# Performance work log

Hardware: AMD Instinct MI355X
Metric: run time of the kernel (lower is better)

The kernel has to match this reference:

```python
import jax, jax.numpy as jnp
import numpy as np

N, E, D_IN, H, L, B, D_OUT = 50000, 800000, 128, 128, 3, 512, 64
BN_EPS = 1e-5


def _leaky(v):
    return jax.nn.leaky_relu(v, 0.2)


def _bn_eval(v, g, b):
    # eval-mode BatchNorm1d with running_mean=0, running_var=1
    return g * v * (1.0 / np.sqrt(1.0 + BN_EPS)) + b


def setup_inputs() -> dict:
    key = jax.random.key(0)
    ks = jax.random.split(key, 12)
    s = 0.02  # weight init scale
    return {
        "x": jax.random.normal(ks[0], (N, D_IN), jnp.float32),
        "edge_index": jax.random.randint(ks[1], (2, E), 0, N, jnp.int64),
        "batch": jnp.sort(jax.random.randint(ks[2], (N,), 0, B, jnp.int64)),
        "node_W": jax.random.normal(ks[3], (D_IN, H), jnp.float32) * s,
        "node_b": jnp.zeros((H,), jnp.float32),
        "conv_W1": jax.random.normal(ks[4], (L, H, H), jnp.float32) * s,
        "conv_b1": jnp.zeros((L, H), jnp.float32),
        "conv_g": jnp.ones((L, H), jnp.float32),
        "conv_beta": jnp.zeros((L, H), jnp.float32),
        "conv_W2": jax.random.normal(ks[5], (L, H, H), jnp.float32) * s,
        "conv_b2": jnp.zeros((L, H), jnp.float32),
        "vn_emb": jax.random.normal(ks[6], (1, H), jnp.float32) * s,
        "vn_W1": jax.random.normal(ks[7], (L, H, H), jnp.float32) * s,
        "vn_b1": jnp.zeros((L, H), jnp.float32),
        "vn_W2": jax.random.normal(ks[8], (L, H, H), jnp.float32) * s,
        "vn_b2": jnp.zeros((L, H), jnp.float32),
        "bn_g": jnp.ones((H,), jnp.float32),
        "bn_b": jnp.zeros((H,), jnp.float32),
        "fc_W": jax.random.normal(ks[9], (D_OUT, H), jnp.float32) * s,
        "fc_b": jnp.zeros((D_OUT,), jnp.float32),
    }


def reference(x, edge_index, batch, node_W, node_b, conv_W1, conv_b1, conv_g,
              conv_beta, conv_W2, conv_b2, vn_emb, vn_W1, vn_b1, vn_W2, vn_b2,
              bn_g, bn_b, fc_W, fc_b):
    src, dst = edge_index[0], edge_index[1]
    h = x @ node_W + node_b                              # [N, H]
    vn = jnp.broadcast_to(vn_emb, (B, vn_emb.shape[1]))  # [B, H]
    counts = jax.ops.segment_sum(jnp.ones((h.shape[0],), h.dtype), batch,
                                 num_segments=B)          # [B]
    denom = jnp.maximum(counts, 1.0)[:, None]
    for l in range(L):
        h = h + vn[batch]
        # GINConv (eps=0): mlp((1+eps)*x + sum of neighbor messages)
        agg = jax.ops.segment_sum(h[src], dst, num_segments=h.shape[0])
        z = h + agg
        z = _leaky(z @ conv_W1[l] + conv_b1[l])
        z = _bn_eval(z, conv_g[l], conv_beta[l])
        h = _leaky(z @ conv_W2[l] + conv_b2[l])
        # dropout is identity in eval mode
        vn_update = jax.ops.segment_sum(h, batch, num_segments=B) / denom
        vn = vn + (_leaky(vn_update @ vn_W1[l] + vn_b1[l]) @ vn_W2[l] + vn_b2[l])
    out = jax.ops.segment_sum(h, batch, num_segments=B)   # global_add_pool
    out = _bn_eval(out, bn_g, bn_b)
    return out @ fc_W.T + fc_b                            # [B, D_OUT]
```

## Files before the change

kernel.cpp:

```cpp
#include <hip/hip_runtime.h>
#include <hip/hip_bf16.h>

#define NN 50000
#define NE 800000
#define NB 512
#define WT_S 136
#define WT_M (128 * WT_S)
#define DCAP 64

using u32 = unsigned int;
using u16 = unsigned short;
typedef __attribute__((ext_vector_type(8))) short short8;
typedef __attribute__((ext_vector_type(4))) float f32x4;

constexpr float BNS = 0.9999950000374998f;

__device__ inline u16 f2bf(float f) {
    u32 b = __builtin_bit_cast(u32, f);
    return (u16)((b + 0x7FFFu + ((b >> 16) & 1u)) >> 16);
}
__device__ inline float bf2f(u32 u) {
    return __builtin_bit_cast(float, u << 16);
}
__device__ inline u32 pk2(float a, float b) {
    return (u32)f2bf(a) | ((u32)f2bf(b) << 16);
}

__global__ void k_wprep(const float* __restrict__ nW, const float* __restrict__ cW1,
                        const float* __restrict__ cW2, u16* __restrict__ wt) {
    int idx = blockIdx.x * 256 + threadIdx.x;
    int m = idx >> 14, e = idx & 16383;
    int k = e >> 7, c = e & 127;
    const float* src = m == 0 ? nW : (m <= 3 ? cW1 + (m - 1) * 16384 : cW2 + (m - 4) * 16384);
    wt[m * WT_M + c * WT_S + k] = f2bf(src[e]);
}

__global__ void k_setup(const float* __restrict__ vn_emb, float* __restrict__ vn,
                        u16* __restrict__ vnb, const int* __restrict__ batch,
                        int* __restrict__ bstart, float* __restrict__ counts) {
    int idx = blockIdx.x * 256 + threadIdx.x;
    if (idx < NB * 128) {
        float v = vn_emb[idx & 127];
        vn[idx] = v;
        vnb[idx] = f2bf(v);
    }
    if (idx <= NB) {
        int b = idx;
        int lo = 0, hi = NN;
        while (lo < hi) { int m = (lo + hi) >> 1; if (batch[m] < b) lo = m + 1; else hi = m; }
        bstart[b] = lo;
        if (b < NB) {
            int b1 = b + 1, lo1 = 0, hi1 = NN;
            while (lo1 < hi1) { int m = (lo1 + hi1) >> 1; if (batch[m] < b1) lo1 = m + 1; else hi1 = m; }
            counts[b] = (float)(lo1 - lo);
        }
    }
}

__global__ void k_pcsr(const int* __restrict__ ei, const int* __restrict__ batch,
                       int* __restrict__ deg, u32* __restrict__ nbr) {
    int e = blockIdx.x * 256 + threadIdx.x;
    if (e >= NE) return;
    int src = ei[e];
    int dst = ei[NE + e];
    int pos = atomicAdd(&deg[dst], 1);
    if (pos < DCAP) nbr[(size_t)dst * DCAP + pos] = (u32)src | ((u32)batch[src] << 16);
}

__global__ __launch_bounds__(256) void k_gather(
    const int* __restrict__ deg, const u32* __restrict__ nbr,
    const u16* __restrict__ hb0, const u16* __restrict__ vnb,
    const int* __restrict__ batch, u16* __restrict__ ah, u16* __restrict__ alo) {
    int node = blockIdx.x * 8 + (threadIdx.x >> 5);
    int q = threadIdx.x & 31;
    if (node >= NN) return;
    const uint2* h2 = (const uint2*)hb0;
    const uint2* v2 = (const uint2*)vnb;
    const u32* nb = nbr + (size_t)node * DCAP;
    int n = min(deg[node], DCAP);
    uint2 vd = h2[(size_t)node * 32 + q];
    uint2 wd = v2[(size_t)batch[node] * 32 + q];
    float4 A = {bf2f(vd.x & 0xFFFFu) + bf2f(wd.x & 0xFFFFu),
                bf2f(vd.x >> 16) + bf2f(wd.x >> 16),
                bf2f(vd.y & 0xFFFFu) + bf2f(wd.y & 0xFFFFu),
                bf2f(vd.y >> 16) + bf2f(wd.y >> 16)};
    float4 Bc = {0.f, 0.f, 0.f, 0.f};
    int j = 0;
    for (; j + 3 < n; j += 4) {
        uint4 nn = *(const uint4*)(nb + j);
        uint2 u0 = h2[(size_t)(nn.x & 0xFFFFu) * 32 + q];
        uint2 w0 = v2[(size_t)(nn.x >> 16) * 32 + q];
        uint2 u1 = h2[(size_t)(nn.y & 0xFFFFu) * 32 + q];
        uint2 w1 = v2[(size_t)(nn.y >> 16) * 32 + q];
        uint2 u2 = h2[(size_t)(nn.z & 0xFFFFu) * 32 + q];
        uint2 w2 = v2[(size_t)(nn.z >> 16) * 32 + q];
        uint2 u3 = h2[(size_t)(nn.w & 0xFFFFu) * 32 + q];
        uint2 w3 = v2[(size_t)(nn.w >> 16) * 32 + q];
        A.x += bf2f(u0.x & 0xFFFFu) + bf2f(w0.x & 0xFFFFu);
        A.y += bf2f(u0.x >> 16) + bf2f(w0.x >> 16);
        A.z += bf2f(u0.y & 0xFFFFu) + bf2f(w0.y & 0xFFFFu);
        A.w += bf2f(u0.y >> 16) + bf2f(w0.y >> 16);
        Bc.x += bf2f(u1.x & 0xFFFFu) + bf2f(w1.x & 0xFFFFu);
        Bc.y += bf2f(u1.x >> 16) + bf2f(w1.x >> 16);
        Bc.z += bf2f(u1.y & 0xFFFFu) + bf2f(w1.y & 0xFFFFu);
        Bc.w += bf2f(u1.y >> 16) + bf2f(w1.y >> 16);
        A.x += bf2f(u2.x & 0xFFFFu) + bf2f(w2.x & 0xFFFFu);
        A.y += bf2f(u2.x >> 16) + bf2f(w2.x >> 16);
        A.z += bf2f(u2.y & 0xFFFFu) + bf2f(w2.y & 0xFFFFu);
        A.w += bf2f(u2.y >> 16) + bf2f(w2.y >> 16);
        Bc.x += bf2f(u3.x & 0xFFFFu) + bf2f(w3.x & 0xFFFFu);
        Bc.y += bf2f(u3.x >> 16) + bf2f(w3.x >> 16);
        Bc.z += bf2f(u3.y & 0xFFFFu) + bf2f(w3.y & 0xFFFFu);
        Bc.w += bf2f(u3.y >> 16) + bf2f(w3.y >> 16);
    }
    for (; j < n; ++j) {
        u32 nn = nb[j];
        uint2 u0 = h2[(size_t)(nn & 0xFFFFu) * 32 + q];
        uint2 w0 = v2[(size_t)(nn >> 16) * 32 + q];
        A.x += bf2f(u0.x & 0xFFFFu) + bf2f(w0.x & 0xFFFFu);
        A.y += bf2f(u0.x >> 16) + bf2f(w0.x >> 16);
        A.z += bf2f(u0.y & 0xFFFFu) + bf2f(w0.y & 0xFFFFu);
        A.w += bf2f(u0.y >> 16) + bf2f(w0.y >> 16);
    }
    A.x += Bc.x; A.y += Bc.y; A.z += Bc.z; A.w += Bc.w;
    u16 h0 = f2bf(A.x), h1 = f2bf(A.y), h2_ = f2bf(A.z), h3 = f2bf(A.w);
    ((uint2*)ah)[(size_t)node * 32 + q] =
        make_uint2((u32)h0 | ((u32)h1 << 16), (u32)h2_ | ((u32)h3 << 16));
    ((uint2*)alo)[(size_t)node * 32 + q] =
        make_uint2(pk2(A.x - bf2f(h0), A.y - bf2f(h1)),
                   pk2(A.z - bf2f(h2_), A.w - bf2f(h3)));
}

template <int EPI, int AMODE, bool OBF16>
__global__ __launch_bounds__(512) void k_gemm(
    const void* __restrict__ Ap, const void* __restrict__ Ap2,
    const u16* __restrict__ wt, const float* __restrict__ bias,
    const float* __restrict__ gg, const float* __restrict__ bb,
    void* __restrict__ outp, int nrows) {
    __shared__ u16 sW[WT_M];
    const int t = threadIdx.x;
    {
        const float4* src = (const float4*)wt;
        float4* dst = (float4*)sW;
        for (int i = t; i < WT_M / 8; i += 512) dst[i] = src[i];
    }
    __syncthreads();
    const int lane = t & 63;
    const int w = t >> 6;
    const int rl = lane & 15;
    const int q = lane >> 4;
    const int rbase = blockIdx.x * 256 + w * 32;

    short8 af[2][4], al[2][4];
#pragma unroll
    for (int ri = 0; ri < 2; ++ri) {
        int row = min(rbase + ri * 16 + rl, nrows - 1);
#pragma unroll
        for (int kc = 0; kc < 4; ++kc) {
            if (AMODE == 2) {
                const float* ap = (const float*)Ap + (size_t)row * 128 + kc * 32 + q * 8;
                float4 f0 = *(const float4*)ap;
                float4 f1 = *(const float4*)(ap + 4);
                float fv[8] = {f0.x, f0.y, f0.z, f0.w, f1.x, f1.y, f1.z, f1.w};
                short8 hi, lo;
#pragma unroll
                for (int i = 0; i < 8; ++i) {
                    u16 hv = f2bf(fv[i]);
                    hi[i] = (short)hv;
                    lo[i] = (short)f2bf(fv[i] - bf2f(hv));
                }
                af[ri][kc] = hi;
                al[ri][kc] = lo;
            } else {
                af[ri][kc] = *(const short8*)((const u16*)Ap + (size_t)row * 128 + kc * 32 + q * 8);
                if (AMODE == 1)
                    al[ri][kc] = *(const short8*)((const u16*)Ap2 + (size_t)row * 128 + kc * 32 + q * 8);
            }
        }
    }

#pragma unroll
    for (int ct = 0; ct < 8; ++ct) {
        f32x4 acc0 = {0.f, 0.f, 0.f, 0.f};
        f32x4 acc1 = {0.f, 0.f, 0.f, 0.f};
#pragma unroll
        for (int kc = 0; kc < 4; ++kc) {
            short8 bf = *(const short8*)&sW[(ct * 16 + rl) * WT_S + kc * 32 + q * 8];
            if (AMODE != 0) {
                acc0 = __builtin_amdgcn_mfma_f32_16x16x32_bf16(al[0][kc], bf, acc0, 0, 0, 0);
                acc1 = __builtin_amdgcn_mfma_f32_16x16x32_bf16(al[1][kc], bf, acc1, 0, 0, 0);
            }
            acc0 = __builtin_amdgcn_mfma_f32_16x16x32_bf16(af[0][kc], bf, acc0, 0, 0, 0);
            acc1 = __builtin_amdgcn_mfma_f32_16x16x32_bf16(af[1][kc], bf, acc1, 0, 0, 0);
        }
        const int col = ct * 16 + rl;
        const float bs = bias[col];
        const float g = (EPI == 2) ? gg[col] : 0.f;
        const float be = (EPI == 2) ? bb[col] : 0.f;
#pragma unroll
        for (int half = 0; half < 2; ++half) {
            const f32x4& ac = half ? acc1 : acc0;
#pragma unroll
            for (int i = 0; i < 4; ++i) {
                int r = rbase + half * 16 + q * 4 + i;
                if (r < nrows) {
                    float v = ac[i] + bs;
                    if (EPI >= 1) v = v > 0.f ? v : 0.2f * v;
                    if (EPI == 2) v = g * v * BNS + be;
                    if (OBF16) ((u16*)outp)[(size_t)r * 128 + col] = f2bf(v);
                    else ((float*)outp)[(size_t)r * 128 + col] = v;
                }
            }
        }
    }
}

__global__ __launch_bounds__(256) void k_vnup(
    const u16* __restrict__ hb0, const int* __restrict__ bstart,
    const float* __restrict__ counts, const float* __restrict__ W1,
    const float* __restrict__ b1, const float* __restrict__ W2,
    const float* __restrict__ b2, float* __restrict__ vn, u16* __restrict__ vnb) {
    __shared__ float4 red[8][32];
    __shared__ float sP[128], sT[128], sH[2][128];
    const int b = blockIdx.x;
    const int t = threadIdx.x;
    const int s = bstart[b], e = bstart[b + 1];
    const int g = t >> 5, q = t & 31;
    const uint2* h2 = (const uint2*)hb0;
    float4 a = make_float4(0.f, 0.f, 0.f, 0.f);
    for (int r = s + g; r < e; r += 8) {
        uint2 v = h2[(size_t)r * 32 + q];
        a.x += bf2f(v.x & 0xFFFFu); a.y += bf2f(v.x >> 16);
        a.z += bf2f(v.y & 0xFFFFu); a.w += bf2f(v.y >> 16);
    }
    red[g][q] = a;
    __syncthreads();
    if (g == 0) {
#pragma unroll
        for (int g2 = 1; g2 < 8; ++g2) {
            float4 v = red[g2][q];
            a.x += v.x; a.y += v.y; a.z += v.z; a.w += v.w;
        }
        float inv = 1.f / fmaxf(counts[b], 1.f);
        sP[q * 4 + 0] = a.x * inv;
        sP[q * 4 + 1] = a.y * inv;
        sP[q * 4 + 2] = a.z * inv;
        sP[q * 4 + 3] = a.w * inv;
    }
    __syncthreads();
    {
        const int c = t & 127, hf = t >> 7;
        float acc = 0.f;
        const float* Wp = W1 + (size_t)(hf * 64) * 128 + c;
#pragma unroll 8
        for (int k = 0; k < 64; ++k) acc += sP[hf * 64 + k] * Wp[(size_t)k * 128];
        sH[hf][c] = acc;
    }
    __syncthreads();
    if (t < 128) {
        float v = sH[0][t] + sH[1][t] + b1[t];
        sT[t] = v > 0.f ? v : 0.2f * v;
    }
    __syncthreads();
    {
        const int c = t & 127, hf = t >> 7;
        float acc = 0.f;
        const float* Wp = W2 + (size_t)(hf * 64) * 128 + c;
#pragma unroll 8
        for (int k = 0; k < 64; ++k) acc += sT[hf * 64 + k] * Wp[(size_t)k * 128];
        sH[hf][c] = acc;
    }
    __syncthreads();
    if (t < 128) {
        float nv = vn[(size_t)b * 128 + t] + sH[0][t] + sH[1][t] + b2[t];
        vn[(size_t)b * 128 + t] = nv;
        vnb[(size_t)b * 128 + t] = f2bf(nv);
    }
}

__global__ __launch_bounds__(256) void k_final(
    const u16* __restrict__ hb0, const int* __restrict__ bstart,
    const float* __restrict__ g, const float* __restrict__ bB,
    const float* __restrict__ fcW, const float* __restrict__ fcb,
    float* __restrict__ out) {
    __shared__ float sP[4][128];
    __shared__ float4 red[4][2][32];
    const int t = threadIdx.x;
    const int seg = t >> 6, gq = t & 63, rg = gq >> 5, q = gq & 31;
    const int b = blockIdx.x * 4 + seg;
    const int s = bstart[b], e = bstart[b + 1];
    const uint2* h2 = (const uint2*)hb0;
    float4 a = make_float4(0.f, 0.f, 0.f, 0.f);
    for (int r = s + rg; r < e; r += 2) {
        uint2 v = h2[(size_t)r * 32 + q];
        a.x += bf2f(v.x & 0xFFFFu); a.y += bf2f(v.x >> 16);
        a.z += bf2f(v.y & 0xFFFFu); a.w += bf2f(v.y >> 16);
    }
    red[seg][rg][q] = a;
    __syncthreads();
    if (rg == 0) {
        float4 v = red[seg][1][q];
        a.x += v.x; a.y += v.y; a.z += v.z; a.w += v.w;
        float av[4] = {a.x, a.y, a.z, a.w};
#pragma unroll
        for (int i = 0; i < 4; ++i) {
            int c = q * 4 + i;
            sP[seg][c] = g[c] * av[i] * BNS + bB[c];
        }
    }
    __syncthreads();
    const int o = t & 63;
    float acc = fcb[o];
    const float* wrow = fcW + o * 128;
    const float* prow = sP[seg];
    for (int k = 0; k < 128; ++k) acc += prow[k] * wrow[k];
    out[(size_t)b * 64 + o] = acc;
}

extern "C" void kernel_launch(void* const* d_in, const int* in_sizes, int n_in,
                              void* d_out, int out_size, void* d_ws, size_t ws_size,
                              hipStream_t stream) {
    const float* x       = (const float*)d_in[0];
    const int*   ei      = (const int*)d_in[1];
    const int*   batch   = (const int*)d_in[2];
    const float* node_W  = (const float*)d_in[3];
    const float* node_b  = (const float*)d_in[4];
    const float* conv_W1 = (const float*)d_in[5];
    const float* conv_b1 = (const float*)d_in[6];
    const float* conv_g  = (const float*)d_in[7];
    const float* conv_bt = (const float*)d_in[8];
    const float* conv_W2 = (const float*)d_in[9];
    const float* conv_b2 = (const float*)d_in[10];
    const float* vn_emb  = (const float*)d_in[11];
    const float* vn_W1   = (const float*)d_in[12];
    const float* vn_b1   = (const float*)d_in[13];
    const float* vn_W2   = (const float*)d_in[14];
    const float* vn_b2   = (const float*)d_in[15];
    const float* bn_g    = (const float*)d_in[16];
    const float* bn_b    = (const float*)d_in[17];
    const float* fc_W    = (const float*)d_in[18];
    const float* fc_b    = (const float*)d_in[19];
    float* out = (float*)d_out;

    char* ws = (char*)d_ws;
    u16* hb0   = (u16*)ws;
    u16* aggh  = hb0 + (size_t)NN * 128;
    u16* agglo = aggh + (size_t)NN * 128;
    u16* wt    = agglo + (size_t)NN * 128;
    u32* nbr   = (u32*)(wt + 7 * WT_M);
    float* vn  = (float*)(nbr + (size_t)NN * DCAP);
    u16* vnb   = (u16*)(vn + NB * 128);
    float* counts = (float*)(vnb + NB * 128);
    int* bstart = (int*)(counts + NB);
    int* deg    = bstart + NB + 1;

    hipMemsetAsync(deg, 0, NN * sizeof(int), stream);
    k_wprep<<<448, 256, 0, stream>>>(node_W, conv_W1, conv_W2, wt);
    k_pcsr<<<(NE + 255) / 256, 256, 0, stream>>>(ei, batch, deg, nbr);
    k_setup<<<(NB * 128 + 255) / 256, 256, 0, stream>>>(vn_emb, vn, vnb, batch, bstart, counts);

    const int GG = (NN + 255) / 256;

    k_gemm<0, 2, true><<<GG, 512, 0, stream>>>(
        x, nullptr, wt, node_b, nullptr, nullptr, hb0, NN);

    for (int l = 0; l < 3; ++l) {
        k_gather<<<(NN + 7) / 8, 256, 0, stream>>>(deg, nbr, hb0, vnb, batch, aggh, agglo);
        k_gemm<2, 1, true><<<GG, 512, 0, stream>>>(
            aggh, agglo, wt + (size_t)(1 + l) * WT_M, conv_b1 + l * 128,
            conv_g + l * 128, conv_bt + l * 128, aggh, NN);
        k_gemm<1, 0, true><<<GG, 512, 0, stream>>>(
            aggh, nullptr, wt + (size_t)(4 + l) * WT_M, conv_b2 + l * 128,
            nullptr, nullptr, hb0, NN);
        if (l < 2)
            k_vnup<<<NB, 256, 0, stream>>>(hb0, bstart, counts, vn_W1 + l * 16384,
                                           vn_b1 + l * 128, vn_W2 + l * 16384,
                                           vn_b2 + l * 128, vn, vnb);
    }

    k_final<<<NB / 4, 256, 0, stream>>>(hb0, bstart, bn_g, bn_b, fc_W, fc_b, out);
}
```

Baseline: 348.0 us.

## Partition edges by destination slice before building padded neighbor lists

Replaces the single scattered CSR build with a two-pass partition. Edges are first bucketed into 8 destination slices using block histograms, a scan and a scatter. A fill kernel then processes each slice with its own group of blocks, so the deg atomics and nbr writes stay within a localized region intended to be cache friendly. The weight-prep and setup kernels are also merged into one launch. This adds three extra launches and an extra pass over the edges. The fill order is also tied to the slice-to-block mapping, which may interact with L2/XCD locality.

After: 358.6 us. 3.0% more time.

```diff
diff --git a/kernel.cpp b/kernel.cpp
--- a/kernel.cpp
+++ b/kernel.cpp
@@ -7,6 +7,11 @@
 #define WT_S 136
 #define WT_M (128 * WT_S)
 #define DCAP 64
+#define NSL 8
+#define SLW 6250
+#define PCH 2048
+#define PBK ((NE + PCH - 1) / PCH)
+#define BPS 112
 
 using u32 = unsigned int;
 using u16 = unsigned short;
@@ -26,19 +31,20 @@
     return (u32)f2bf(a) | ((u32)f2bf(b) << 16);
 }
 
-__global__ void k_wprep(const float* __restrict__ nW, const float* __restrict__ cW1,
-                        const float* __restrict__ cW2, u16* __restrict__ wt) {
-    int idx = blockIdx.x * 256 + threadIdx.x;
-    int m = idx >> 14, e = idx & 16383;
-    int k = e >> 7, c = e & 127;
-    const float* src = m == 0 ? nW : (m <= 3 ? cW1 + (m - 1) * 16384 : cW2 + (m - 4) * 16384);
-    wt[m * WT_M + c * WT_S + k] = f2bf(src[e]);
-}
-
-__global__ void k_setup(const float* __restrict__ vn_emb, float* __restrict__ vn,
-                        u16* __restrict__ vnb, const int* __restrict__ batch,
-                        int* __restrict__ bstart, float* __restrict__ counts) {
-    int idx = blockIdx.x * 256 + threadIdx.x;
+__global__ void k_prep(const float* __restrict__ nW, const float* __restrict__ cW1,
+                       const float* __restrict__ cW2, u16* __restrict__ wt,
+                       const float* __restrict__ vn_emb, float* __restrict__ vn,
+                       u16* __restrict__ vnb, const int* __restrict__ batch,
+                       int* __restrict__ bstart, float* __restrict__ counts) {
+    if (blockIdx.x < 448) {
+        int idx = blockIdx.x * 256 + threadIdx.x;
+        int m = idx >> 14, e = idx & 16383;
+        int k = e >> 7, c = e & 127;
+        const float* src = m == 0 ? nW : (m <= 3 ? cW1 + (m - 1) * 16384 : cW2 + (m - 4) * 16384);
+        wt[m * WT_M + c * WT_S + k] = f2bf(src[e]);
+        return;
+    }
+    int idx = (blockIdx.x - 448) * 256 + threadIdx.x;
     if (idx < NB * 128) {
         float v = vn_emb[idx & 127];
         vn[idx] = v;
@@ -57,14 +63,82 @@
     }
 }
 
-__global__ void k_pcsr(const int* __restrict__ ei, const int* __restrict__ batch,
-                       int* __restrict__ deg, u32* __restrict__ nbr) {
-    int e = blockIdx.x * 256 + threadIdx.x;
-    if (e >= NE) return;
-    int src = ei[e];
-    int dst = ei[NE + e];
-    int pos = atomicAdd(&deg[dst], 1);
-    if (pos < DCAP) nbr[(size_t)dst * DCAP + pos] = (u32)src | ((u32)batch[src] << 16);
+__global__ __launch_bounds__(256) void k_part1(const int* __restrict__ ei,
+                                               int* __restrict__ blkcnt) {
+    __shared__ int hist[NSL];
+    const int t = threadIdx.x;
+    if (t < NSL) hist[t] = 0;
+    __syncthreads();
+    int base = blockIdx.x * PCH + t * 8;
+#pragma unroll
+    for (int i = 0; i < 8; ++i) {
+        int e = base + i;
+        if (e < NE) atomicAdd(&hist[ei[NE + e] / SLW], 1);
+    }
+    __syncthreads();
+    if (t < NSL) blkcnt[t * PBK + blockIdx.x] = hist[t];
+}
+
+__global__ __launch_bounds__(512) void k_pscan(const int* __restrict__ blkcnt,
+                                               int* __restrict__ blkofs,
+                                               int* __restrict__ sinfo) {
+    __shared__ int s[NSL * PBK];
+    __shared__ int tot[NSL], gb[NSL];
+    const int t = threadIdx.x;
+    for (int i = t; i < NSL * PBK; i += 512) s[i] = blkcnt[i];
+    __syncthreads();
+    if (t < NSL) {
+        int run = 0;
+        for (int b = 0; b < PBK; ++b) { int v = s[t * PBK + b]; s[t * PBK + b] = run; run += v; }
+        tot[t] = run;
+    }
+    __syncthreads();
+    if (t == 0) {
+        int run = 0;
+        for (int i = 0; i < NSL; ++i) { gb[i] = run; run += tot[i]; }
+    }
+    __syncthreads();
+    for (int i = t; i < NSL * PBK; i += 512) blkofs[i] = gb[i / PBK] + s[i];
+    if (t < NSL) { sinfo[t] = gb[t]; sinfo[NSL + t] = tot[t]; }
+}
+
+__global__ __launch_bounds__(256) void k_part2(const int* __restrict__ ei,
+                                               const int* __restrict__ blkofs,
+                                               u32* __restrict__ part) {
+    __shared__ int cur[NSL];
+    const int t = threadIdx.x;
+    if (t < NSL) cur[t] = blkofs[t * PBK + blockIdx.x];
+    __syncthreads();
+    int base = blockIdx.x * PCH + t * 8;
+#pragma unroll
+    for (int i = 0; i < 8; ++i) {
+        int e = base + i;
+        if (e < NE) {
+            int dst = ei[NE + e];
+            int src = ei[e];
+            int sl = dst / SLW;
+            int pos = atomicAdd(&cur[sl], 1);
+            part[pos] = (u32)src | ((u32)(dst - sl * SLW) << 16);
+        }
+    }
+}
+
+__global__ __launch_bounds__(256) void k_pfill(const u32* __restrict__ part,
+                                               const int* __restrict__ sinfo,
+                                               const int* __restrict__ batch,
+                                               int* __restrict__ deg, u32* __restrict__ nbr) {
+    const int sl = blockIdx.x & (NSL - 1);
+    const int sub = blockIdx.x >> 3;
+    const int base = sinfo[sl], cnt = sinfo[NSL + sl];
+    const int chunk = (cnt + BPS - 1) / BPS;
+    const int lo = sub * chunk, hi = min(lo + chunk, cnt);
+    for (int i = lo + (int)threadIdx.x; i < hi; i += 256) {
+        u32 v = part[base + i];
+        int src = (int)(v & 0xFFFFu);
+        int dst = sl * SLW + (int)(v >> 16);
+        int pos = atomicAdd(&deg[dst], 1);
+        if (pos < DCAP) nbr[(size_t)dst * DCAP + pos] = (u32)src | ((u32)batch[src] << 16);
+    }
 }
 
 __global__ __launch_bounds__(256) void k_gather(
@@ -348,16 +422,23 @@
     u16* agglo = aggh + (size_t)NN * 128;
     u16* wt    = agglo + (size_t)NN * 128;
     u32* nbr   = (u32*)(wt + 7 * WT_M);
-    float* vn  = (float*)(nbr + (size_t)NN * DCAP);
+    u32* part  = nbr + (size_t)NN * DCAP;
+    int* blkcnt = (int*)(part + NE);
+    int* blkofs = blkcnt + NSL * PBK;
+    int* sinfo  = blkofs + NSL * PBK;
+    float* vn  = (float*)(sinfo + 2 * NSL);
     u16* vnb   = (u16*)(vn + NB * 128);
     float* counts = (float*)(vnb + NB * 128);
     int* bstart = (int*)(counts + NB);
     int* deg    = bstart + NB + 1;
 
     hipMemsetAsync(deg, 0, NN * sizeof(int), stream);
-    k_wprep<<<448, 256, 0, stream>>>(node_W, conv_W1, conv_W2, wt);
-    k_pcsr<<<(NE + 255) / 256, 256, 0, stream>>>(ei, batch, deg, nbr);
-    k_setup<<<(NB * 128 + 255) / 256, 256, 0, stream>>>(vn_emb, vn, vnb, batch, bstart, counts);
+    k_prep<<<704, 256, 0, stream>>>(node_W, conv_W1, conv_W2, wt,
+                                    vn_emb, vn, vnb, batch, bstart, counts);
+    k_part1<<<PBK, 256, 0, stream>>>(ei, blkcnt);
+    k_pscan<<<1, 512, 0, stream>>>(blkcnt, blkofs, sinfo);
+    k_part2<<<PBK, 256, 0, stream>>>(ei, blkofs, part);
+    k_pfill<<<NSL * BPS, 256, 0, stream>>>(part, sinfo, batch, deg, nbr);
 
     const int GG = (NN + 255) / 256;
 
```

## Store node features in feature-sliced layout and partition gather by slice for cache locality

Applied to the files above, without the earlier changes.

Node embeddings and virtual-node embeddings are stored transposed into four 32-feature slices, so each slice of all nodes is contiguous. The gather kernel is restructured so each block handles one feature slice for half the nodes, with two lanes splitting the neighbor list and combining through a shuffle. This aims to shrink the working set per pass so random neighbor reads hit in L2/MALL. The setup and weight-prep kernels are also merged into one launch. The GEMM epilogue now writes scattered 2-byte stores into the sliced layout, which costs some write coalescing.

Result: slower. 365.9 us, median of 3 (+5.1%).

```diff
diff --git a/kernel.cpp b/kernel.cpp
--- a/kernel.cpp
+++ b/kernel.cpp
@@ -4,6 +4,7 @@
 #define NN 50000
 #define NE 800000
 #define NB 512
+#define HNN 25000
 #define WT_S 136
 #define WT_M (128 * WT_S)
 #define DCAP 64
@@ -26,23 +27,26 @@
     return (u32)f2bf(a) | ((u32)f2bf(b) << 16);
 }
 
-__global__ void k_wprep(const float* __restrict__ nW, const float* __restrict__ cW1,
-                        const float* __restrict__ cW2, u16* __restrict__ wt) {
-    int idx = blockIdx.x * 256 + threadIdx.x;
-    int m = idx >> 14, e = idx & 16383;
-    int k = e >> 7, c = e & 127;
-    const float* src = m == 0 ? nW : (m <= 3 ? cW1 + (m - 1) * 16384 : cW2 + (m - 4) * 16384);
-    wt[m * WT_M + c * WT_S + k] = f2bf(src[e]);
-}
-
-__global__ void k_setup(const float* __restrict__ vn_emb, float* __restrict__ vn,
-                        u16* __restrict__ vnb, const int* __restrict__ batch,
-                        int* __restrict__ bstart, float* __restrict__ counts) {
-    int idx = blockIdx.x * 256 + threadIdx.x;
+
+__global__ void k_prep(const float* __restrict__ nW, const float* __restrict__ cW1,
+                       const float* __restrict__ cW2, u16* __restrict__ wt,
+                       const float* __restrict__ vn_emb, float* __restrict__ vn,
+                       u16* __restrict__ vnbT, const int* __restrict__ batch,
+                       int* __restrict__ bstart, float* __restrict__ counts) {
+    if (blockIdx.x < 448) {
+        int idx = blockIdx.x * 256 + threadIdx.x;
+        int m = idx >> 14, e = idx & 16383;
+        int k = e >> 7, c = e & 127;
+        const float* src = m == 0 ? nW : (m <= 3 ? cW1 + (m - 1) * 16384 : cW2 + (m - 4) * 16384);
+        wt[m * WT_M + c * WT_S + k] = f2bf(src[e]);
+        return;
+    }
+    int idx = (blockIdx.x - 448) * 256 + threadIdx.x;
     if (idx < NB * 128) {
-        float v = vn_emb[idx & 127];
+        int b = idx >> 7, c = idx & 127;
+        float v = vn_emb[c];
         vn[idx] = v;
-        vnb[idx] = f2bf(v);
+        vnbT[((size_t)(c >> 5) * NB + b) * 32 + (c & 31)] = f2bf(v);
     }
     if (idx <= NB) {
         int b = idx;
@@ -69,74 +73,105 @@
 
 __global__ __launch_bounds__(256) void k_gather(
     const int* __restrict__ deg, const u32* __restrict__ nbr,
-    const u16* __restrict__ hb0, const u16* __restrict__ vnb,
+    const u16* __restrict__ hbT, const u16* __restrict__ vnbT,
     const int* __restrict__ batch, u16* __restrict__ ah, u16* __restrict__ alo) {
-    int node = blockIdx.x * 8 + (threadIdx.x >> 5);
-    int q = threadIdx.x & 31;
-    if (node >= NN) return;
-    const uint2* h2 = (const uint2*)hb0;
-    const uint2* v2 = (const uint2*)vnb;
-    const u32* nb = nbr + (size_t)node * DCAP;
-    int n = min(deg[node], DCAP);
-    uint2 vd = h2[(size_t)node * 32 + q];
-    uint2 wd = v2[(size_t)batch[node] * 32 + q];
-    float4 A = {bf2f(vd.x & 0xFFFFu) + bf2f(wd.x & 0xFFFFu),
-                bf2f(vd.x >> 16) + bf2f(wd.x >> 16),
-                bf2f(vd.y & 0xFFFFu) + bf2f(wd.y & 0xFFFFu),
-                bf2f(vd.y >> 16) + bf2f(wd.y >> 16)};
-    float4 Bc = {0.f, 0.f, 0.f, 0.f};
-    int j = 0;
-    for (; j + 3 < n; j += 4) {
-        uint4 nn = *(const uint4*)(nb + j);
-        uint2 u0 = h2[(size_t)(nn.x & 0xFFFFu) * 32 + q];
-        uint2 w0 = v2[(size_t)(nn.x >> 16) * 32 + q];
-        uint2 u1 = h2[(size_t)(nn.y & 0xFFFFu) * 32 + q];
-        uint2 w1 = v2[(size_t)(nn.y >> 16) * 32 + q];
-        uint2 u2 = h2[(size_t)(nn.z & 0xFFFFu) * 32 + q];
-        uint2 w2 = v2[(size_t)(nn.z >> 16) * 32 + q];
-        uint2 u3 = h2[(size_t)(nn.w & 0xFFFFu) * 32 + q];
-        uint2 w3 = v2[(size_t)(nn.w >> 16) * 32 + q];
-        A.x += bf2f(u0.x & 0xFFFFu) + bf2f(w0.x & 0xFFFFu);
-        A.y += bf2f(u0.x >> 16) + bf2f(w0.x >> 16);
-        A.z += bf2f(u0.y & 0xFFFFu) + bf2f(w0.y & 0xFFFFu);
-        A.w += bf2f(u0.y >> 16) + bf2f(w0.y >> 16);
-        Bc.x += bf2f(u1.x & 0xFFFFu) + bf2f(w1.x & 0xFFFFu);
-        Bc.y += bf2f(u1.x >> 16) + bf2f(w1.x >> 16);
-        Bc.z += bf2f(u1.y & 0xFFFFu) + bf2f(w1.y & 0xFFFFu);
-        Bc.w += bf2f(u1.y >> 16) + bf2f(w1.y >> 16);
-        A.x += bf2f(u2.x & 0xFFFFu) + bf2f(w2.x & 0xFFFFu);
-        A.y += bf2f(u2.x >> 16) + bf2f(w2.x >> 16);
-        A.z += bf2f(u2.y & 0xFFFFu) + bf2f(w2.y & 0xFFFFu);
-        A.w += bf2f(u2.y >> 16) + bf2f(w2.y >> 16);
-        Bc.x += bf2f(u3.x & 0xFFFFu) + bf2f(w3.x & 0xFFFFu);
-        Bc.y += bf2f(u3.x >> 16) + bf2f(w3.x >> 16);
-        Bc.z += bf2f(u3.y & 0xFFFFu) + bf2f(w3.y & 0xFFFFu);
-        Bc.w += bf2f(u3.y >> 16) + bf2f(w3.y >> 16);
-    }
-    for (; j < n; ++j) {
-        u32 nn = nb[j];
-        uint2 u0 = h2[(size_t)(nn & 0xFFFFu) * 32 + q];
-        uint2 w0 = v2[(size_t)(nn >> 16) * 32 + q];
-        A.x += bf2f(u0.x & 0xFFFFu) + bf2f(w0.x & 0xFFFFu);
-        A.y += bf2f(u0.x >> 16) + bf2f(w0.x >> 16);
-        A.z += bf2f(u0.y & 0xFFFFu) + bf2f(w0.y & 0xFFFFu);
-        A.w += bf2f(u0.y >> 16) + bf2f(w0.y >> 16);
-    }
-    A.x += Bc.x; A.y += Bc.y; A.z += Bc.z; A.w += Bc.w;
-    u16 h0 = f2bf(A.x), h1 = f2bf(A.y), h2_ = f2bf(A.z), h3 = f2bf(A.w);
-    ((uint2*)ah)[(size_t)node * 32 + q] =
-        make_uint2((u32)h0 | ((u32)h1 << 16), (u32)h2_ | ((u32)h3 << 16));
-    ((uint2*)alo)[(size_t)node * 32 + q] =
-        make_uint2(pk2(A.x - bf2f(h0), A.y - bf2f(h1)),
-                   pk2(A.z - bf2f(h2_), A.w - bf2f(h3)));
-}
-
-template <int EPI, int AMODE, bool OBF16>
+    const int s = blockIdx.x & 7;
+    const int sub = blockIdx.x >> 3;
+    const int f = s & 3;
+    const int hs = s >> 2;
+    const int lane = threadIdx.x & 63;
+    const int w = threadIdx.x >> 6;
+    const int g = lane >> 3, sl = lane & 7;
+    const int pair = sl >> 2, fl = sl & 3;
+    const int local = sub * 32 + w * 8 + g;
+    if (local >= HNN) return;
+    const int node = hs * HNN + local;
+
+    const uint4* hT = (const uint4*)hbT + (size_t)f * NN * 4;
+    const uint4* vT = (const uint4*)vnbT + (size_t)f * NB * 4;
+    const u32* nbp = nbr + (size_t)node * DCAP;
+    const int n = min(deg[node], DCAP);
+
+    float acc[8];
+    if (pair == 0) {
+        uint4 hv = hT[(size_t)node * 4 + fl];
+        uint4 vv = vT[(size_t)batch[node] * 4 + fl];
+        acc[0] = bf2f(hv.x & 0xFFFFu) + bf2f(vv.x & 0xFFFFu);
+        acc[1] = bf2f(hv.x >> 16) + bf2f(vv.x >> 16);
+        acc[2] = bf2f(hv.y & 0xFFFFu) + bf2f(vv.y & 0xFFFFu);
+        acc[3] = bf2f(hv.y >> 16) + bf2f(vv.y >> 16);
+        acc[4] = bf2f(hv.z & 0xFFFFu) + bf2f(vv.z & 0xFFFFu);
+        acc[5] = bf2f(hv.z >> 16) + bf2f(vv.z >> 16);
+        acc[6] = bf2f(hv.w & 0xFFFFu) + bf2f(vv.w & 0xFFFFu);
+        acc[7] = bf2f(hv.w >> 16) + bf2f(vv.w >> 16);
+    } else {
+#pragma unroll
+        for (int i = 0; i < 8; ++i) acc[i] = 0.f;
+    }
+
+    int j = pair;
+    for (; j + 2 < n; j += 4) {
+        u32 e0 = nbp[j], e1 = nbp[j + 2];
+        uint4 h0 = hT[(size_t)(e0 & 0xFFFFu) * 4 + fl];
+        uint4 v0 = vT[(size_t)(e0 >> 16) * 4 + fl];
+        uint4 h1 = hT[(size_t)(e1 & 0xFFFFu) * 4 + fl];
+        uint4 v1 = vT[(size_t)(e1 >> 16) * 4 + fl];
+        acc[0] += bf2f(h0.x & 0xFFFFu) + bf2f(v0.x & 0xFFFFu);
+        acc[1] += bf2f(h0.x >> 16) + bf2f(v0.x >> 16);
+        acc[2] += bf2f(h0.y & 0xFFFFu) + bf2f(v0.y & 0xFFFFu);
+        acc[3] += bf2f(h0.y >> 16) + bf2f(v0.y >> 16);
+        acc[4] += bf2f(h0.z & 0xFFFFu) + bf2f(v0.z & 0xFFFFu);
+        acc[5] += bf2f(h0.z >> 16) + bf2f(v0.z >> 16);
+        acc[6] += bf2f(h0.w & 0xFFFFu) + bf2f(v0.w & 0xFFFFu);
+        acc[7] += bf2f(h0.w >> 16) + bf2f(v0.w >> 16);
+        acc[0] += bf2f(h1.x & 0xFFFFu) + bf2f(v1.x & 0xFFFFu);
+        acc[1] += bf2f(h1.x >> 16) + bf2f(v1.x >> 16);
+        acc[2] += bf2f(h1.y & 0xFFFFu) + bf2f(v1.y & 0xFFFFu);
+        acc[3] += bf2f(h1.y >> 16) + bf2f(v1.y >> 16);
+        acc[4] += bf2f(h1.z & 0xFFFFu) + bf2f(v1.z & 0xFFFFu);
+        acc[5] += bf2f(h1.z >> 16) + bf2f(v1.z >> 16);
+        acc[6] += bf2f(h1.w & 0xFFFFu) + bf2f(v1.w & 0xFFFFu);
+        acc[7] += bf2f(h1.w >> 16) + bf2f(v1.w >> 16);
+    }
+    if (j < n) {
+        u32 e0 = nbp[j];
+        uint4 h0 = hT[(size_t)(e0 & 0xFFFFu) * 4 + fl];
+        uint4 v0 = vT[(size_t)(e0 >> 16) * 4 + fl];
+        acc[0] += bf2f(h0.x & 0xFFFFu) + bf2f(v0.x & 0xFFFFu);
+        acc[1] += bf2f(h0.x >> 16) + bf2f(v0.x >> 16);
+        acc[2] += bf2f(h0.y & 0xFFFFu) + bf2f(v0.y & 0xFFFFu);
+        acc[3] += bf2f(h0.y >> 16) + bf2f(v0.y >> 16);
+        acc[4] += bf2f(h0.z & 0xFFFFu) + bf2f(v0.z & 0xFFFFu);
+        acc[5] += bf2f(h0.z >> 16) + bf2f(v0.z >> 16);
+        acc[6] += bf2f(h0.w & 0xFFFFu) + bf2f(v0.w & 0xFFFFu);
+        acc[7] += bf2f(h0.w >> 16) + bf2f(v0.w >> 16);
+    }
+
+#pragma unroll
+    for (int i = 0; i < 8; ++i) acc[i] += __shfl_xor(acc[i], 4);
+
+    if (pair == 0) {
+        u16 hi[8];
+#pragma unroll
+        for (int i = 0; i < 8; ++i) hi[i] = f2bf(acc[i]);
+        uint4 ho = {(u32)hi[0] | ((u32)hi[1] << 16), (u32)hi[2] | ((u32)hi[3] << 16),
+                    (u32)hi[4] | ((u32)hi[5] << 16), (u32)hi[6] | ((u32)hi[7] << 16)};
+        uint4 lo = {pk2(acc[0] - bf2f(hi[0]), acc[1] - bf2f(hi[1])),
+                    pk2(acc[2] - bf2f(hi[2]), acc[3] - bf2f(hi[3])),
+                    pk2(acc[4] - bf2f(hi[4]), acc[5] - bf2f(hi[5])),
+                    pk2(acc[6] - bf2f(hi[6]), acc[7] - bf2f(hi[7]))};
+        const size_t oi = (size_t)node * 16 + f * 4 + fl;
+        ((uint4*)ah)[oi] = ho;
+        ((uint4*)alo)[oi] = lo;
+    }
+}
+
+template <int EPI, int AMODE, int OMODE>
 __global__ __launch_bounds__(512) void k_gemm(
     const void* __restrict__ Ap, const void* __restrict__ Ap2,
     const u16* __restrict__ wt, const float* __restrict__ bias,
     const float* __restrict__ gg, const float* __restrict__ bb,
-    void* __restrict__ outp, int nrows) {
+    u16* __restrict__ outp, int nrows) {
     __shared__ u16 sW[WT_M];
     const int t = threadIdx.x;
     {
@@ -207,8 +242,10 @@
                     float v = ac[i] + bs;
                     if (EPI >= 1) v = v > 0.f ? v : 0.2f * v;
                     if (EPI == 2) v = g * v * BNS + be;
-                    if (OBF16) ((u16*)outp)[(size_t)r * 128 + col] = f2bf(v);
-                    else ((float*)outp)[(size_t)r * 128 + col] = v;
+                    if (OMODE == 0)
+                        outp[(size_t)r * 128 + col] = f2bf(v);
+                    else
+                        outp[((size_t)(col >> 5) * NN + r) * 32 + (col & 31)] = f2bf(v);
                 }
             }
         }
@@ -216,20 +253,22 @@
 }
 
 __global__ __launch_bounds__(256) void k_vnup(
-    const u16* __restrict__ hb0, const int* __restrict__ bstart,
+    const u16* __restrict__ hbT, const int* __restrict__ bstart,
     const float* __restrict__ counts, const float* __restrict__ W1,
     const float* __restrict__ b1, const float* __restrict__ W2,
-    const float* __restrict__ b2, float* __restrict__ vn, u16* __restrict__ vnb) {
+    const float* __restrict__ b2, float* __restrict__ vn, u16* __restrict__ vnbT) {
     __shared__ float4 red[8][32];
     __shared__ float sP[128], sT[128], sH[2][128];
     const int b = blockIdx.x;
     const int t = threadIdx.x;
     const int s = bstart[b], e = bstart[b + 1];
     const int g = t >> 5, q = t & 31;
-    const uint2* h2 = (const uint2*)hb0;
+    const uint2* h2 = (const uint2*)hbT;
+    const size_t fbase = (size_t)(q >> 3) * NN * 8;
+    const int fo = q & 7;
     float4 a = make_float4(0.f, 0.f, 0.f, 0.f);
     for (int r = s + g; r < e; r += 8) {
-        uint2 v = h2[(size_t)r * 32 + q];
+        uint2 v = h2[fbase + (size_t)r * 8 + fo];
         a.x += bf2f(v.x & 0xFFFFu); a.y += bf2f(v.x >> 16);
         a.z += bf2f(v.y & 0xFFFFu); a.w += bf2f(v.y >> 16);
     }
@@ -274,12 +313,12 @@
     if (t < 128) {
         float nv = vn[(size_t)b * 128 + t] + sH[0][t] + sH[1][t] + b2[t];
         vn[(size_t)b * 128 + t] = nv;
-        vnb[(size_t)b * 128 + t] = f2bf(nv);
+        vnbT[((size_t)(t >> 5) * NB + b) * 32 + (t & 31)] = f2bf(nv);
     }
 }
 
 __global__ __launch_bounds__(256) void k_final(
-    const u16* __restrict__ hb0, const int* __restrict__ bstart,
+    const u16* __restrict__ hbT, const int* __restrict__ bstart,
     const float* __restrict__ g, const float* __restrict__ bB,
     const float* __restrict__ fcW, const float* __restrict__ fcb,
     float* __restrict__ out) {
@@ -289,10 +328,12 @@
     const int seg = t >> 6, gq = t & 63, rg = gq >> 5, q = gq & 31;
     const int b = blockIdx.x * 4 + seg;
     const int s = bstart[b], e = bstart[b + 1];
-    const uint2* h2 = (const uint2*)hb0;
+    const uint2* h2 = (const uint2*)hbT;
+    const size_t fbase = (size_t)(q >> 3) * NN * 8;
+    const int fo = q & 7;
     float4 a = make_float4(0.f, 0.f, 0.f, 0.f);
     for (int r = s + rg; r < e; r += 2) {
-        uint2 v = h2[(size_t)r * 32 + q];
+        uint2 v = h2[fbase + (size_t)r * 8 + fo];
         a.x += bf2f(v.x & 0xFFFFu); a.y += bf2f(v.x >> 16);
         a.z += bf2f(v.y & 0xFFFFu); a.w += bf2f(v.y >> 16);
     }
@@ -343,40 +384,41 @@
     float* out = (float*)d_out;
 
     char* ws = (char*)d_ws;
-    u16* hb0   = (u16*)ws;
-    u16* aggh  = hb0 + (size_t)NN * 128;
+    u16* hbT   = (u16*)ws;
+    u16* aggh  = hbT + (size_t)NN * 128;
     u16* agglo = aggh + (size_t)NN * 128;
     u16* wt    = agglo + (size_t)NN * 128;
     u32* nbr   = (u32*)(wt + 7 * WT_M);
     float* vn  = (float*)(nbr + (size_t)NN * DCAP);
-    u16* vnb   = (u16*)(vn + NB * 128);
-    float* counts = (float*)(vnb + NB * 128);
+    u16* vnbT  = (u16*)(vn + NB * 128);
+    float* counts = (float*)(vnbT + NB * 128);
     int* bstart = (int*)(counts + NB);
     int* deg    = bstart + NB + 1;
 
     hipMemsetAsync(deg, 0, NN * sizeof(int), stream);
-    k_wprep<<<448, 256, 0, stream>>>(node_W, conv_W1, conv_W2, wt);
+    k_prep<<<704, 256, 0, stream>>>(node_W, conv_W1, conv_W2, wt,
+                                    vn_emb, vn, vnbT, batch, bstart, counts);
     k_pcsr<<<(NE + 255) / 256, 256, 0, stream>>>(ei, batch, deg, nbr);
-    k_setup<<<(NB * 128 + 255) / 256, 256, 0, stream>>>(vn_emb, vn, vnb, batch, bstart, counts);
 
     const int GG = (NN + 255) / 256;
-
-    k_gemm<0, 2, true><<<GG, 512, 0, stream>>>(
-        x, nullptr, wt, node_b, nullptr, nullptr, hb0, NN);
+    const int GGA = 8 * ((HNN + 31) / 32);
+
+    k_gemm<0, 2, 1><<<GG, 512, 0, stream>>>(
+        x, nullptr, wt, node_b, nullptr, nullptr, hbT, NN);
 
     for (int l = 0; l < 3; ++l) {
-        k_gather<<<(NN + 7) / 8, 256, 0, stream>>>(deg, nbr, hb0, vnb, batch, aggh, agglo);
-        k_gemm<2, 1, true><<<GG, 512, 0, stream>>>(
+        k_gather<<<GGA, 256, 0, stream>>>(deg, nbr, hbT, vnbT, batch, aggh, agglo);
+        k_gemm<2, 1, 0><<<GG, 512, 0, stream>>>(
             aggh, agglo, wt + (size_t)(1 + l) * WT_M, conv_b1 + l * 128,
             conv_g + l * 128, conv_bt + l * 128, aggh, NN);
-        k_gemm<1, 0, true><<<GG, 512, 0, stream>>>(
+        k_gemm<1, 0, 1><<<GG, 512, 0, stream>>>(
             aggh, nullptr, wt + (size_t)(4 + l) * WT_M, conv_b2 + l * 128,
-            nullptr, nullptr, hb0, NN);
+            nullptr, nullptr, hbT, NN);
         if (l < 2)
-            k_vnup<<<NB, 256, 0, stream>>>(hb0, bstart, counts, vn_W1 + l * 16384,
+            k_vnup<<<NB, 256, 0, stream>>>(hbT, bstart, counts, vn_W1 + l * 16384,
                                            vn_b1 + l * 128, vn_W2 + l * 16384,
-                                           vn_b2 + l * 128, vn, vnb);
-    }
-
-    k_final<<<NB / 4, 256, 0, stream>>>(hb0, bstart, bn_g, bn_b, fc_W, fc_b, out);
-}
+                                           vn_b2 + l * 128, vn, vnbT);
+    }
+
+    k_final<<<NB / 4, 256, 0, stream>>>(hbT, bstart, bn_g, bn_b, fc_W, fc_b, out);
+}
```

## Split neighbor-list build into per-XCD edge segments with smaller per-segment capacity

Applied to the files above, without the earlier changes.

The padded adjacency build is split into 8 edge segments. Each segment keeps its own degree counters and a 16-slot neighbor list per node, so that atomics and writes for a segment stay in one block group, likely one per XCD, which cuts cross-die atomic contention. The gather kernel loops over all 8 segment lists per node. The weight-prep and setup kernels are merged into one launch. The layout raises nbr and deg memory and adds per-node degree reads in the gather, and a node with more than 16 in-edges from one segment would silently drop neighbors.

New measurement: 444.0 us. 1.28x slower.

```diff
diff --git a/kernel.cpp b/kernel.cpp
--- a/kernel.cpp
+++ b/kernel.cpp
@@ -6,7 +6,10 @@
 #define NB 512
 #define WT_S 136
 #define WT_M (128 * WT_S)
-#define DCAP 64
+#define NSEG 8
+#define DCAP2 16
+#define CHK (NE / NSEG)
+#define BPS 96
 
 using u32 = unsigned int;
 using u16 = unsigned short;
@@ -26,19 +29,20 @@
     return (u32)f2bf(a) | ((u32)f2bf(b) << 16);
 }
 
-__global__ void k_wprep(const float* __restrict__ nW, const float* __restrict__ cW1,
-                        const float* __restrict__ cW2, u16* __restrict__ wt) {
-    int idx = blockIdx.x * 256 + threadIdx.x;
-    int m = idx >> 14, e = idx & 16383;
-    int k = e >> 7, c = e & 127;
-    const float* src = m == 0 ? nW : (m <= 3 ? cW1 + (m - 1) * 16384 : cW2 + (m - 4) * 16384);
-    wt[m * WT_M + c * WT_S + k] = f2bf(src[e]);
-}
-
-__global__ void k_setup(const float* __restrict__ vn_emb, float* __restrict__ vn,
-                        u16* __restrict__ vnb, const int* __restrict__ batch,
-                        int* __restrict__ bstart, float* __restrict__ counts) {
-    int idx = blockIdx.x * 256 + threadIdx.x;
+__global__ void k_prep(const float* __restrict__ nW, const float* __restrict__ cW1,
+                       const float* __restrict__ cW2, u16* __restrict__ wt,
+                       const float* __restrict__ vn_emb, float* __restrict__ vn,
+                       u16* __restrict__ vnb, const int* __restrict__ batch,
+                       int* __restrict__ bstart, float* __restrict__ counts) {
+    if (blockIdx.x < 448) {
+        int idx = blockIdx.x * 256 + threadIdx.x;
+        int m = idx >> 14, e = idx & 16383;
+        int k = e >> 7, c = e & 127;
+        const float* src = m == 0 ? nW : (m <= 3 ? cW1 + (m - 1) * 16384 : cW2 + (m - 4) * 16384);
+        wt[m * WT_M + c * WT_S + k] = f2bf(src[e]);
+        return;
+    }
+    int idx = (blockIdx.x - 448) * 256 + threadIdx.x;
     if (idx < NB * 128) {
         float v = vn_emb[idx & 127];
         vn[idx] = v;
@@ -59,12 +63,16 @@
 
 __global__ void k_pcsr(const int* __restrict__ ei, const int* __restrict__ batch,
                        int* __restrict__ deg, u32* __restrict__ nbr) {
-    int e = blockIdx.x * 256 + threadIdx.x;
-    if (e >= NE) return;
-    int src = ei[e];
-    int dst = ei[NE + e];
-    int pos = atomicAdd(&deg[dst], 1);
-    if (pos < DCAP) nbr[(size_t)dst * DCAP + pos] = (u32)src | ((u32)batch[src] << 16);
+    const int x = blockIdx.x & (NSEG - 1);
+    const int sub = blockIdx.x >> 3;
+    const int lo = x * CHK, hi = lo + CHK;
+    for (int e = lo + sub * 256 + (int)threadIdx.x; e < hi; e += BPS * 256) {
+        int src = ei[e];
+        int dst = ei[NE + e];
+        int pos = atomicAdd(&deg[x * NN + dst], 1);
+        if (pos < DCAP2)
+            nbr[((size_t)x * NN + dst) * DCAP2 + pos] = (u32)src | ((u32)batch[src] << 16);
+    }
 }
 
 __global__ __launch_bounds__(256) void k_gather(
@@ -76,8 +84,6 @@
     if (node >= NN) return;
     const uint2* h2 = (const uint2*)hb0;
     const uint2* v2 = (const uint2*)vnb;
-    const u32* nb = nbr + (size_t)node * DCAP;
-    int n = min(deg[node], DCAP);
     uint2 vd = h2[(size_t)node * 32 + q];
     uint2 wd = v2[(size_t)batch[node] * 32 + q];
     float4 A = {bf2f(vd.x & 0xFFFFu) + bf2f(wd.x & 0xFFFFu),
@@ -85,42 +91,35 @@
                 bf2f(vd.y & 0xFFFFu) + bf2f(wd.y & 0xFFFFu),
                 bf2f(vd.y >> 16) + bf2f(wd.y >> 16)};
     float4 Bc = {0.f, 0.f, 0.f, 0.f};
-    int j = 0;
-    for (; j + 3 < n; j += 4) {
-        uint4 nn = *(const uint4*)(nb + j);
-        uint2 u0 = h2[(size_t)(nn.x & 0xFFFFu) * 32 + q];
-        uint2 w0 = v2[(size_t)(nn.x >> 16) * 32 + q];
-        uint2 u1 = h2[(size_t)(nn.y & 0xFFFFu) * 32 + q];
-        uint2 w1 = v2[(size_t)(nn.y >> 16) * 32 + q];
-        uint2 u2 = h2[(size_t)(nn.z & 0xFFFFu) * 32 + q];
-        uint2 w2 = v2[(size_t)(nn.z >> 16) * 32 + q];
-        uint2 u3 = h2[(size_t)(nn.w & 0xFFFFu) * 32 + q];
-        uint2 w3 = v2[(size_t)(nn.w >> 16) * 32 + q];
-        A.x += bf2f(u0.x & 0xFFFFu) + bf2f(w0.x & 0xFFFFu);
-        A.y += bf2f(u0.x >> 16) + bf2f(w0.x >> 16);
-        A.z += bf2f(u0.y & 0xFFFFu) + bf2f(w0.y & 0xFFFFu);
-        A.w += bf2f(u0.y >> 16) + bf2f(w0.y >> 16);
-        Bc.x += bf2f(u1.x & 0xFFFFu) + bf2f(w1.x & 0xFFFFu);
-        Bc.y += bf2f(u1.x >> 16) + bf2f(w1.x >> 16);
-        Bc.z += bf2f(u1.y & 0xFFFFu) + bf2f(w1.y & 0xFFFFu);
-        Bc.w += bf2f(u1.y >> 16) + bf2f(w1.y >> 16);
-        A.x += bf2f(u2.x & 0xFFFFu) + bf2f(w2.x & 0xFFFFu);
-        A.y += bf2f(u2.x >> 16) + bf2f(w2.x >> 16);
-        A.z += bf2f(u2.y & 0xFFFFu) + bf2f(w2.y & 0xFFFFu);
-        A.w += bf2f(u2.y >> 16) + bf2f(w2.y >> 16);
-        Bc.x += bf2f(u3.x & 0xFFFFu) + bf2f(w3.x & 0xFFFFu);
-        Bc.y += bf2f(u3.x >> 16) + bf2f(w3.x >> 16);
-        Bc.z += bf2f(u3.y & 0xFFFFu) + bf2f(w3.y & 0xFFFFu);
-        Bc.w += bf2f(u3.y >> 16) + bf2f(w3.y >> 16);
-    }
-    for (; j < n; ++j) {
-        u32 nn = nb[j];
-        uint2 u0 = h2[(size_t)(nn & 0xFFFFu) * 32 + q];
-        uint2 w0 = v2[(size_t)(nn >> 16) * 32 + q];
-        A.x += bf2f(u0.x & 0xFFFFu) + bf2f(w0.x & 0xFFFFu);
-        A.y += bf2f(u0.x >> 16) + bf2f(w0.x >> 16);
-        A.z += bf2f(u0.y & 0xFFFFu) + bf2f(w0.y & 0xFFFFu);
-        A.w += bf2f(u0.y >> 16) + bf2f(w0.y >> 16);
+#pragma unroll
+    for (int x = 0; x < NSEG; ++x) {
+        int n = min(deg[x * NN + node], DCAP2);
+        const u32* nbp = nbr + ((size_t)x * NN + node) * DCAP2;
+        int j = 0;
+        for (; j + 1 < n; j += 2) {
+            u32 e0 = nbp[j], e1 = nbp[j + 1];
+            uint2 u0 = h2[(size_t)(e0 & 0xFFFFu) * 32 + q];
+            uint2 w0 = v2[(size_t)(e0 >> 16) * 32 + q];
+            uint2 u1 = h2[(size_t)(e1 & 0xFFFFu) * 32 + q];
+            uint2 w1 = v2[(size_t)(e1 >> 16) * 32 + q];
+            A.x += bf2f(u0.x & 0xFFFFu) + bf2f(w0.x & 0xFFFFu);
+            A.y += bf2f(u0.x >> 16) + bf2f(w0.x >> 16);
+            A.z += bf2f(u0.y & 0xFFFFu) + bf2f(w0.y & 0xFFFFu);
+            A.w += bf2f(u0.y >> 16) + bf2f(w0.y >> 16);
+            Bc.x += bf2f(u1.x & 0xFFFFu) + bf2f(w1.x & 0xFFFFu);
+            Bc.y += bf2f(u1.x >> 16) + bf2f(w1.x >> 16);
+            Bc.z += bf2f(u1.y & 0xFFFFu) + bf2f(w1.y & 0xFFFFu);
+            Bc.w += bf2f(u1.y >> 16) + bf2f(w1.y >> 16);
+        }
+        if (j < n) {
+            u32 e0 = nbp[j];
+            uint2 u0 = h2[(size_t)(e0 & 0xFFFFu) * 32 + q];
+            uint2 w0 = v2[(size_t)(e0 >> 16) * 32 + q];
+            A.x += bf2f(u0.x & 0xFFFFu) + bf2f(w0.x & 0xFFFFu);
+            A.y += bf2f(u0.x >> 16) + bf2f(w0.x >> 16);
+            A.z += bf2f(u0.y & 0xFFFFu) + bf2f(w0.y & 0xFFFFu);
+            A.w += bf2f(u0.y >> 16) + bf2f(w0.y >> 16);
+        }
     }
     A.x += Bc.x; A.y += Bc.y; A.z += Bc.z; A.w += Bc.w;
     u16 h0 = f2bf(A.x), h1 = f2bf(A.y), h2_ = f2bf(A.z), h3 = f2bf(A.w);
@@ -131,12 +130,12 @@
                    pk2(A.z - bf2f(h2_), A.w - bf2f(h3)));
 }
 
-template <int EPI, int AMODE, bool OBF16>
+template <int EPI, int AMODE>
 __global__ __launch_bounds__(512) void k_gemm(
     const void* __restrict__ Ap, const void* __restrict__ Ap2,
     const u16* __restrict__ wt, const float* __restrict__ bias,
     const float* __restrict__ gg, const float* __restrict__ bb,
-    void* __restrict__ outp, int nrows) {
+    u16* __restrict__ outp, int nrows) {
     __shared__ u16 sW[WT_M];
     const int t = threadIdx.x;
     {
@@ -207,8 +206,7 @@
                     float v = ac[i] + bs;
                     if (EPI >= 1) v = v > 0.f ? v : 0.2f * v;
                     if (EPI == 2) v = g * v * BNS + be;
-                    if (OBF16) ((u16*)outp)[(size_t)r * 128 + col] = f2bf(v);
-                    else ((float*)outp)[(size_t)r * 128 + col] = v;
+                    outp[(size_t)r * 128 + col] = f2bf(v);
                 }
             }
         }
@@ -348,28 +346,28 @@
     u16* agglo = aggh + (size_t)NN * 128;
     u16* wt    = agglo + (size_t)NN * 128;
     u32* nbr   = (u32*)(wt + 7 * WT_M);
-    float* vn  = (float*)(nbr + (size_t)NN * DCAP);
+    float* vn  = (float*)(nbr + (size_t)NSEG * NN * DCAP2);
     u16* vnb   = (u16*)(vn + NB * 128);
     float* counts = (float*)(vnb + NB * 128);
     int* bstart = (int*)(counts + NB);
     int* deg    = bstart + NB + 1;
 
-    hipMemsetAsync(deg, 0, NN * sizeof(int), stream);
-    k_wprep<<<448, 256, 0, stream>>>(node_W, conv_W1, conv_W2, wt);
-    k_pcsr<<<(NE + 255) / 256, 256, 0, stream>>>(ei, batch, deg, nbr);
-    k_setup<<<(NB * 128 + 255) / 256, 256, 0, stream>>>(vn_emb, vn, vnb, batch, bstart, counts);
+    hipMemsetAsync(deg, 0, (size_t)NSEG * NN * sizeof(int), stream);
+    k_prep<<<704, 256, 0, stream>>>(node_W, conv_W1, conv_W2, wt,
+                                    vn_emb, vn, vnb, batch, bstart, counts);
+    k_pcsr<<<NSEG * BPS, 256, 0, stream>>>(ei, batch, deg, nbr);
 
     const int GG = (NN + 255) / 256;
 
-    k_gemm<0, 2, true><<<GG, 512, 0, stream>>>(
+    k_gemm<0, 2><<<GG, 512, 0, stream>>>(
         x, nullptr, wt, node_b, nullptr, nullptr, hb0, NN);
 
     for (int l = 0; l < 3; ++l) {
         k_gather<<<(NN + 7) / 8, 256, 0, stream>>>(deg, nbr, hb0, vnb, batch, aggh, agglo);
-        k_gemm<2, 1, true><<<GG, 512, 0, stream>>>(
+        k_gemm<2, 1><<<GG, 512, 0, stream>>>(
             aggh, agglo, wt + (size_t)(1 + l) * WT_M, conv_b1 + l * 128,
             conv_g + l * 128, conv_bt + l * 128, aggh, NN);
-        k_gemm<1, 0, true><<<GG, 512, 0, stream>>>(
+        k_gemm<1, 0><<<GG, 512, 0, stream>>>(
             aggh, nullptr, wt + (size_t)(4 + l) * WT_M, conv_b2 + l * 128,
             nullptr, nullptr, hb0, NN);
         if (l < 2)
```
